# Performance work log

Hardware: AMD Instinct MI355X
Metric: run time of the kernel (lower is better)

The kernel has to match this reference:

```python
import jax, jax.numpy as jnp
import numpy as np

D_MODEL = 2048
NUM_HEADS = 16
HEAD_DIM = D_MODEL // NUM_HEADS


def setup_inputs() -> dict:
    key = jax.random.key(0)
    ks = jax.random.split(key, 11)
    B, S = 2, 2048
    scale = 1.0 / np.sqrt(D_MODEL)
    inp = {
        "q": jax.random.normal(ks[0], (B, S, D_MODEL), jnp.float32),
        "k": jax.random.normal(ks[1], (B, S, D_MODEL), jnp.float32),
        "v": jax.random.normal(ks[2], (B, S, D_MODEL), jnp.float32),
        "Wq": jax.random.normal(ks[3], (D_MODEL, D_MODEL), jnp.float32) * scale,
        "bq": jnp.zeros((D_MODEL,), jnp.float32),
        "Wk": jax.random.normal(ks[4], (D_MODEL, D_MODEL), jnp.float32) * scale,
        "bk": jnp.zeros((D_MODEL,), jnp.float32),
        "Wv": jax.random.normal(ks[5], (D_MODEL, D_MODEL), jnp.float32) * scale,
        "bv": jnp.zeros((D_MODEL,), jnp.float32),
        "Wo": jax.random.normal(ks[6], (D_MODEL, D_MODEL), jnp.float32) * scale,
        "bo": jnp.zeros((D_MODEL,), jnp.float32),
    }
    return inp


def reference(q, k, v, Wq, bq, Wk, bk, Wv, bv, Wo, bo):
    B, S, _ = q.shape
    # projections (torch Linear: x @ W.T + b)
    qh = (q @ Wq.T + bq).reshape(B, S, NUM_HEADS, HEAD_DIM).transpose(0, 2, 1, 3)
    kh = (k @ Wk.T + bk).reshape(B, S, NUM_HEADS, HEAD_DIM).transpose(0, 2, 1, 3)
    vh = (v @ Wv.T + bv).reshape(B, S, NUM_HEADS, HEAD_DIM).transpose(0, 2, 1, 3)
    # scaled dot-product attention, full O(S^2) scores as in original
    scores = jnp.einsum("bhqd,bhkd->bhqk", qh, kh) / jnp.sqrt(
        jnp.asarray(HEAD_DIM, jnp.float32)
    )
    attn = jax.nn.softmax(scores, axis=-1)
    out = jnp.einsum("bhqk,bhkd->bhqd", attn, vh)
    out = out.transpose(0, 2, 1, 3).reshape(B, S, D_MODEL)
    return out @ Wo.T + bo
```

## Files before the change

### kernel.cpp

```cpp
#include <hip/hip_runtime.h>


typedef __attribute__((ext_vector_type(8))) short bf16x8;
typedef __attribute__((ext_vector_type(4))) float f32x4;
typedef __attribute__((ext_vector_type(8))) unsigned short u16x8;

__device__ __forceinline__ unsigned short f2bf(float f) {
  unsigned int u = __float_as_uint(f);
  u += 0x7fffu + ((u >> 16) & 1u);
  return (unsigned short)(u >> 16);
}

#if __has_builtin(__builtin_amdgcn_cvt_pk_bf16_f32)
__device__ __forceinline__ unsigned int pack2bf(float x, float y) {
  auto r = __builtin_amdgcn_cvt_pk_bf16_f32(x, y);
  return __builtin_bit_cast(unsigned int, r);
}
#else
__device__ __forceinline__ unsigned int pack2bf(float x, float y) {
  return (unsigned int)f2bf(x) | ((unsigned int)f2bf(y) << 16);
}
#endif

__device__ __forceinline__ float fast_exp2(float x) {
#if __has_builtin(__builtin_amdgcn_exp2f)
  return __builtin_amdgcn_exp2f(x);
#else
  return exp2f(x);
#endif
}

__device__ __forceinline__ void async16(const void* g, void* l) {
  __builtin_amdgcn_global_load_lds(
      (const __attribute__((address_space(1))) unsigned int*)g,
      (__attribute__((address_space(3))) unsigned int*)l, 16, 0, 0);
}

__device__ __forceinline__ f32x4 mfma_bf16(bf16x8 a, bf16x8 b, f32x4 c) {
  return __builtin_amdgcn_mfma_f32_16x16x32_bf16(a, b, c, 0, 0, 0);
}

__global__ __launch_bounds__(256) void cvt_kernel(
    const float* __restrict__ q, const float* __restrict__ k,
    const float* __restrict__ v, const float* __restrict__ Wq,
    const float* __restrict__ Wk, const float* __restrict__ Wv,
    const float* __restrict__ Wo, unsigned short* __restrict__ Xq,
    unsigned short* __restrict__ Xk, unsigned short* __restrict__ Xv,
    unsigned short* __restrict__ WqB, unsigned short* __restrict__ WkB,
    unsigned short* __restrict__ WvB, unsigned short* __restrict__ WoB) {
  size_t i = ((size_t)blockIdx.x * 256 + threadIdx.x) * 8;
  const float* src;
  unsigned short* dst;
  size_t off;
  if (i < 8388608ull) { src = q; dst = Xq; off = i; }
  else if (i < 16777216ull) { src = k; dst = Xk; off = i - 8388608ull; }
  else if (i < 25165824ull) { src = v; dst = Xv; off = i - 16777216ull; }
  else if (i < 29360128ull) { src = Wq; dst = WqB; off = i - 25165824ull; }
  else if (i < 33554432ull) { src = Wk; dst = WkB; off = i - 29360128ull; }
  else if (i < 37748736ull) { src = Wv; dst = WvB; off = i - 33554432ull; }
  else { src = Wo; dst = WoB; off = i - 37748736ull; }
  f32x4 a = *(const f32x4*)(src + off);
  f32x4 b = *(const f32x4*)(src + off + 4);
  u16x8 r;
  r[0] = f2bf(a[0]); r[1] = f2bf(a[1]); r[2] = f2bf(a[2]); r[3] = f2bf(a[3]);
  r[4] = f2bf(b[0]); r[5] = f2bf(b[1]); r[6] = f2bf(b[2]); r[7] = f2bf(b[3]);
  *(u16x8*)(dst + off) = r;
}

#define MFMA_PHASE(AF, MB)                                                    \
  do {                                                                        \
    __builtin_amdgcn_s_setprio(1);                                            \
    _Pragma("unroll") for (int ks = 0; ks < 2; ++ks) {                        \
      _Pragma("unroll") for (int m2 = 0; m2 < 2; ++m2) {                      \
        _Pragma("unroll") for (int nt = 0; nt < 4; ++nt) {                    \
          acc[(MB) + m2][nt] =                                                \
              mfma_bf16(AF[m2][ks], Bf[nt][ks], acc[(MB) + m2][nt]);          \
        }                                                                     \
      }                                                                       \
    }                                                                         \
    __builtin_amdgcn_s_setprio(0);                                            \
  } while (0)

__global__ __launch_bounds__(512, 2) void qkv_gemm256(
    const unsigned short* __restrict__ Xq, const unsigned short* __restrict__ Xk,
    const unsigned short* __restrict__ Xv, const unsigned short* __restrict__ Wq,
    const unsigned short* __restrict__ Wk, const unsigned short* __restrict__ Wv,
    const float* __restrict__ bq, const float* __restrict__ bk,
    const float* __restrict__ bv, unsigned short* __restrict__ Qb,
    unsigned short* __restrict__ Kb, unsigned short* __restrict__ Vt) {
  __shared__ unsigned short S[2][4][128 * 64];
  const int z = blockIdx.z;
  const unsigned short* A = z == 0 ? Xq : z == 1 ? Xk : Xv;
  const unsigned short* Bm = z == 0 ? Wq : z == 1 ? Wk : Wv;
  const float* bias = z == 0 ? bq : z == 1 ? bk : bv;
  const int m0 = blockIdx.y * 256;
  const int n0 = blockIdx.x * 256;
  const int tid = threadIdx.x;
  const int lane = tid & 63;
  const int wave = tid >> 6;
  const int quad = lane >> 4;
  const int l15 = lane & 15;
  const int wm = wave >> 2;
  const int wn = wave & 3;
  const int cxor = l15 & 7;
  const int K = 2048;

  auto stage = [&](int r, int kt, int buf) {
#pragma unroll
    for (int p = 0; p < 2; ++p) {
      int x = p * 512 + tid;
      int row = ((x >> 7) << 4) + ((x >> 3) & 15);
      int gk = kt * 64 + (((x & 7) ^ ((x >> 3) & 7)) << 3);
      const unsigned short* src =
          (r < 2) ? Bm + (size_t)(n0 + r * 128 + row) * K + gk
                  : A + (size_t)(m0 + (r - 2) * 128 + row) * K + gk;
      async16(src, (char*)S[buf][r] + (size_t)(p * 512 + wave * 64) * 16);
    }
  };
  auto rdA = [&](int buf, int mt, int ks) -> bf16x8 {
    const unsigned short* base = S[buf][2 + wm];
    int chunk = mt * 128 + l15 * 8 + ((ks * 4 + quad) ^ cxor);
    return *(const bf16x8*)(base + chunk * 8);
  };
  auto rdB = [&](int buf, int nt, int ks) -> bf16x8 {
    const unsigned short* base = S[buf][wn >> 1];
    int chunk = ((wn & 1) * 4 + nt) * 128 + l15 * 8 + ((ks * 4 + quad) ^ cxor);
    return *(const bf16x8*)(base + chunk * 8);
  };

  f32x4 acc[8][4];
#pragma unroll
  for (int i = 0; i < 8; ++i)
#pragma unroll
    for (int j = 0; j < 4; ++j) acc[i][j] = f32x4{0.f, 0.f, 0.f, 0.f};
  bf16x8 Bf[4][2], AX[2][2], AY[2][2];

  stage(0, 0, 0); stage(1, 0, 0); stage(2, 0, 0); stage(3, 0, 0);
  stage(0, 1, 1); stage(1, 1, 1); stage(2, 1, 1);
  asm volatile("s_waitcnt vmcnt(6)" ::: "memory");
  __builtin_amdgcn_s_barrier();
#pragma unroll
  for (int nt = 0; nt < 4; ++nt)
#pragma unroll
    for (int ks = 0; ks < 2; ++ks) Bf[nt][ks] = rdB(0, nt, ks);
#pragma unroll
  for (int ks = 0; ks < 2; ++ks) {
    AX[0][ks] = rdA(0, 0, ks);
    AX[1][ks] = rdA(0, 1, ks);
  }

#pragma unroll 1
  for (int t = 0; t < 32; ++t) {
    const int buf = t & 1;
    const int nbuf = buf ^ 1;
    if (t < 31) stage(3, t + 1, nbuf);
#pragma unroll
    for (int ks = 0; ks < 2; ++ks) {
      AY[0][ks] = rdA(buf, 2, ks);
      AY[1][ks] = rdA(buf, 3, ks);
    }
    __builtin_amdgcn_sched_barrier(0);
    __builtin_amdgcn_s_barrier();
    __builtin_amdgcn_sched_barrier(0);
    MFMA_PHASE(AX, 0);
    __builtin_amdgcn_sched_barrier(0);
    __builtin_amdgcn_s_barrier();
    if (t < 30) stage(0, t + 2, buf);
#pragma unroll
    for (int ks = 0; ks < 2; ++ks) {
      AX[0][ks] = rdA(buf, 4, ks);
      AX[1][ks] = rdA(buf, 5, ks);
    }
    __builtin_amdgcn_sched_barrier(0);
    __builtin_amdgcn_s_barrier();
    __builtin_amdgcn_sched_barrier(0);
    MFMA_PHASE(AY, 2);
    __builtin_amdgcn_sched_barrier(0);
    __builtin_amdgcn_s_barrier();
    if (t < 30) stage(1, t + 2, buf);
#pragma unroll
    for (int ks = 0; ks < 2; ++ks) {
      AY[0][ks] = rdA(buf, 6, ks);
      AY[1][ks] = rdA(buf, 7, ks);
    }
    __builtin_amdgcn_sched_barrier(0);
    __builtin_amdgcn_s_barrier();
    __builtin_amdgcn_sched_barrier(0);
    MFMA_PHASE(AX, 4);
    if (t < 30) {
      asm volatile("s_waitcnt vmcnt(4)" ::: "memory");
    } else if (t == 30) {
      asm volatile("s_waitcnt vmcnt(0)" ::: "memory");
    }
    __builtin_amdgcn_sched_barrier(0);
    __builtin_amdgcn_s_barrier();
    if (t < 30) stage(2, t + 2, buf);
    if (t < 31) {
#pragma unroll
      for (int ks = 0; ks < 2; ++ks) {
        AX[0][ks] = rdA(nbuf, 0, ks);
        AX[1][ks] = rdA(nbuf, 1, ks);
      }
    }
    __builtin_amdgcn_sched_barrier(0);
    __builtin_amdgcn_s_barrier();
    __builtin_amdgcn_sched_barrier(0);
    MFMA_PHASE(AY, 6);
    if (t < 31) {
#pragma unroll
      for (int nt = 0; nt < 4; ++nt)
#pragma unroll
        for (int ks = 0; ks < 2; ++ks) Bf[nt][ks] = rdB(nbuf, nt, ks);
    }
    __builtin_amdgcn_sched_barrier(0);
    __builtin_amdgcn_s_barrier();
  }

  const float SK = z == 0 ? 0.12753102331285527f : 1.0f;
#pragma unroll
  for (int nt = 0; nt < 4; ++nt) {
    int col = n0 + wn * 64 + nt * 16 + l15;
    float bv_ = bias[col];
    if (z == 2) {
      int h = col >> 7, d = col & 127;
#pragma unroll
      for (int mt = 0; mt < 8; ++mt) {
        int row0 = m0 + wm * 128 + mt * 16 + quad * 4;
        int bb = row0 >> 11, s = row0 & 2047;
        uint2 pk;
        pk.x = pack2bf(acc[mt][nt][0] + bv_, acc[mt][nt][1] + bv_);
        pk.y = pack2bf(acc[mt][nt][2] + bv_, acc[mt][nt][3] + bv_);
        *(uint2*)(Vt + ((size_t)((bb * 16 + h) * 128 + d)) * 2048 + s) = pk;
      }
    } else {
      unsigned short* C = z == 0 ? Qb : Kb;
#pragma unroll
      for (int mt = 0; mt < 8; ++mt) {
        int row0 = m0 + wm * 128 + mt * 16 + quad * 4;
#pragma unroll
        for (int r = 0; r < 4; ++r)
          C[(size_t)(row0 + r) * 2048 + col] = f2bf((acc[mt][nt][r] + bv_) * SK);
      }
    }
  }
}

__device__ __forceinline__ void gemm_core_k2048(
    const unsigned short* __restrict__ A, const unsigned short* __restrict__ Bm,
    int m0, int n0, unsigned short* As, unsigned short* Bs,
    f32x4 (&acc)[4][4]) {
  const int tid = threadIdx.x;
  const int lane = tid & 63;
  const int wave = tid >> 6;
  const int quad = lane >> 4;
  const int l15 = lane & 15;
  const int wmt = (wave >> 1) * 4;
  const int wnt = (wave & 1) * 4;
  const int K = 2048;

  auto stage = [&](int kt, int buf) {
    unsigned short* SA = As + buf * (128 * 64);
    unsigned short* SB = Bs + buf * (128 * 64);
#pragma unroll
    for (int p = 0; p < 4; ++p) {
      int x = p * 256 + tid;
      int row = ((x >> 7) << 4) + ((x >> 3) & 15);
      int gk = kt + (((x & 7) ^ ((x >> 3) & 7)) << 3);
      async16(A + (size_t)(m0 + row) * K + gk,
              (char*)SA + (size_t)(p * 256 + wave * 64) * 16);
      async16(Bm + (size_t)(n0 + row) * K + gk,
              (char*)SB + (size_t)(p * 256 + wave * 64) * 16);
    }
  };
  stage(0, 0);
#pragma unroll 1
  for (int it = 0; it < 32; ++it) {
    __syncthreads();
    if (it + 1 < 32) stage((it + 1) * 64, (it + 1) & 1);
    const unsigned short* SA = As + (it & 1) * (128 * 64);
    const unsigned short* SB = Bs + (it & 1) * (128 * 64);
#pragma unroll
    for (int s = 0; s < 2; ++s) {
      const int cs = (s * 4 + quad) ^ (l15 & 7);
      bf16x8 af[4], bfr[4];
#pragma unroll
      for (int t = 0; t < 4; ++t) {
        af[t] = *(const bf16x8*)(SA + ((wmt + t) * 128 + l15 * 8 + cs) * 8);
        bfr[t] = *(const bf16x8*)(SB + ((wnt + t) * 128 + l15 * 8 + cs) * 8);
      }
#pragma unroll
      for (int mt = 0; mt < 4; ++mt)
#pragma unroll
        for (int nt = 0; nt < 4; ++nt)
          acc[mt][nt] = mfma_bf16(af[mt], bfr[nt], acc[mt][nt]);
    }
  }
}

__global__ __launch_bounds__(256, 2) void o_gemm(
    const unsigned short* __restrict__ A, const unsigned short* __restrict__ Bm,
    const float* __restrict__ bias, float* __restrict__ Cf) {
  __shared__ unsigned short As[2][128 * 64];
  __shared__ unsigned short Bs[2][128 * 64];
  const int m0 = blockIdx.y * 128;
  const int n0 = blockIdx.x * 128;

  f32x4 acc[4][4];
#pragma unroll
  for (int i = 0; i < 4; ++i)
#pragma unroll
    for (int j = 0; j < 4; ++j) acc[i][j] = f32x4{0.f, 0.f, 0.f, 0.f};
  gemm_core_k2048(A, Bm, m0, n0, As[0], Bs[0], acc);

  const int lane = threadIdx.x & 63;
  const int wave = threadIdx.x >> 6;
  const int quad = lane >> 4;
  const int l15 = lane & 15;
  const int wmt = (wave >> 1) * 4;
  const int wnt = (wave & 1) * 4;
  const int N = 2048;
#pragma unroll
  for (int nt = 0; nt < 4; ++nt) {
    int col = n0 + (wnt + nt) * 16 + l15;
    float bv_ = bias[col];
#pragma unroll
    for (int mt = 0; mt < 4; ++mt) {
      int row0 = m0 + (wmt + mt) * 16 + quad * 4;
#pragma unroll
      for (int r = 0; r < 4; ++r)
        Cf[(size_t)(row0 + r) * N + col] = acc[mt][nt][r] + bv_;
    }
  }
}

__global__ __launch_bounds__(256, 2) void attn_kernel(
    const unsigned short* __restrict__ Qg, const unsigned short* __restrict__ Kg,
    const unsigned short* __restrict__ Vt, unsigned short* __restrict__ ctx) {
  __shared__ unsigned short Ks[2][64 * 128];
  __shared__ unsigned short Vs[2][128 * 64];
  __shared__ unsigned short Ps[128 * 64];
  const int tid = threadIdx.x;
  const int lane = tid & 63;
  const int wave = tid >> 6;
  const int quad = lane >> 4;
  const int l15 = lane & 15;
  const int qt = blockIdx.x, h = blockIdx.y, b = blockIdx.z;
  const int q0 = qt * 128;
  const int swz = (l15 & 7) * 8;

  bf16x8 aq[2][4];
#pragma unroll
  for (int mt = 0; mt < 2; ++mt) {
    const unsigned short* qrow =
        Qg + (size_t)(b * 2048 + q0 + wave * 32 + mt * 16 + l15) * 2048 + h * 128;
#pragma unroll
    for (int ks = 0; ks < 4; ++ks)
      aq[mt][ks] = *(const bf16x8*)(qrow + ks * 32 + quad * 8);
  }

  f32x4 o[2][8];
#pragma unroll
  for (int mt = 0; mt < 2; ++mt)
#pragma unroll
    for (int dt = 0; dt < 8; ++dt) o[mt][dt] = f32x4{0.f, 0.f, 0.f, 0.f};
  f32x4 lacc[2] = {f32x4{0.f, 0.f, 0.f, 0.f}, f32x4{0.f, 0.f, 0.f, 0.f}};

  auto stage = [&](int t, int buf) {
#pragma unroll
    for (int p = 0; p < 4; ++p) {
      int slot = p * 256 + tid;
      {
        int nt = slot >> 8, c = (slot >> 4) & 15, r15 = slot & 15;
        const unsigned short* g =
            Kg + (size_t)(b * 2048 + t * 64 + nt * 16 + r15) * 2048 + h * 128 + c * 8;
        async16(g, (char*)Ks[buf] + (size_t)(p * 256 + wave * 64) * 16);
      }
      {
        int dt = slot >> 7, c = (slot >> 4) & 7, n15 = slot & 15;
        const unsigned short* g =
            Vt + ((size_t)(b * 16 + h) * 128 + dt * 16 + n15) * 2048 + t * 64 + c * 8;
        async16(g, (char*)Vs[buf] + (size_t)(p * 256 + wave * 64) * 16);
      }
    }
  };
  stage(0, 0);

  for (int t = 0; t < 32; ++t) {
    __syncthreads();
    if (t + 1 < 32) stage(t + 1, (t + 1) & 1);
    const unsigned short* Kb = Ks[t & 1];
    const unsigned short* Vb = Vs[t & 1];

    f32x4 sc[2][4];
#pragma unroll
    for (int nt = 0; nt < 4; ++nt) {
      sc[0][nt] = f32x4{0.f, 0.f, 0.f, 0.f};
      sc[1][nt] = f32x4{0.f, 0.f, 0.f, 0.f};
#pragma unroll
      for (int ks = 0; ks < 4; ++ks) {
        bf16x8 bk = *(const bf16x8*)(Kb + (nt * 256 + (ks * 4 + quad) * 16 + l15) * 8);
        sc[0][nt] = mfma_bf16(bk, aq[0][ks], sc[0][nt]);
        sc[1][nt] = mfma_bf16(bk, aq[1][ks], sc[1][nt]);
      }
    }

#pragma unroll
    for (int mt = 0; mt < 2; ++mt) {
      int prow = (wave * 32 + mt * 16 + l15) * 64;
#pragma unroll
      for (int nt = 0; nt < 4; ++nt) {
        f32x4 p;
#pragma unroll
        for (int r = 0; r < 4; ++r) p[r] = fast_exp2(sc[mt][nt][r]);
        lacc[mt] += p;
        uint2 pk;
        pk.x = pack2bf(p[0], p[1]);
        pk.y = pack2bf(p[2], p[3]);
        *(uint2*)(Ps + prow + ((nt * 16 + quad * 4) ^ swz)) = pk;
      }
    }

    bf16x8 ap[2][2];
#pragma unroll
    for (int mt = 0; mt < 2; ++mt) {
      int prow = (wave * 32 + mt * 16 + l15) * 64;
#pragma unroll
      for (int ks = 0; ks < 2; ++ks)
        ap[mt][ks] = *(const bf16x8*)(Ps + prow + ((ks * 32 + quad * 8) ^ swz));
    }
#pragma unroll
    for (int dt = 0; dt < 8; ++dt) {
#pragma unroll
      for (int ks = 0; ks < 2; ++ks) {
        bf16x8 bv = *(const bf16x8*)(Vb + (dt * 128 + (ks * 4 + quad) * 16 + l15) * 8);
        o[0][dt] = mfma_bf16(ap[0][ks], bv, o[0][dt]);
        o[1][dt] = mfma_bf16(ap[1][ks], bv, o[1][dt]);
      }
    }
  }

  float lq[2];
#pragma unroll
  for (int mt = 0; mt < 2; ++mt) {
    float s = lacc[mt][0] + lacc[mt][1] + lacc[mt][2] + lacc[mt][3];
    s += __shfl_xor(s, 16, 64);
    s += __shfl_xor(s, 32, 64);
    lq[mt] = s;
  }

#pragma unroll
  for (int mt = 0; mt < 2; ++mt) {
#pragma unroll
    for (int r = 0; r < 4; ++r) {
      float lr = __shfl(lq[mt], quad * 4 + r, 64);
      float inv = 1.0f / lr;
      unsigned short* crow =
          ctx + (size_t)(b * 2048 + q0 + wave * 32 + mt * 16 + quad * 4 + r) * 2048 +
          h * 128;
#pragma unroll
      for (int dt = 0; dt < 8; ++dt)
        crow[dt * 16 + l15] = f2bf(o[mt][dt][r] * inv);
    }
  }
}

extern "C" void kernel_launch(void* const* d_in, const int* in_sizes, int n_in,
                              void* d_out, int out_size, void* d_ws,
                              size_t ws_size, hipStream_t stream) {
  const float* q = (const float*)d_in[0];
  const float* k = (const float*)d_in[1];
  const float* v = (const float*)d_in[2];
  const float* Wq = (const float*)d_in[3];
  const float* bq = (const float*)d_in[4];
  const float* Wk = (const float*)d_in[5];
  const float* bk = (const float*)d_in[6];
  const float* Wv = (const float*)d_in[7];
  const float* bv = (const float*)d_in[8];
  const float* Wo = (const float*)d_in[9];
  const float* bo = (const float*)d_in[10];
  float* out = (float*)d_out;

  char* ws = (char*)d_ws;
  const size_t MB = 1024 * 1024;
  unsigned short* Xq  = (unsigned short*)(ws + 0 * MB);
  unsigned short* Xk  = (unsigned short*)(ws + 16 * MB);
  unsigned short* Xv  = (unsigned short*)(ws + 32 * MB);
  unsigned short* WqB = (unsigned short*)(ws + 48 * MB);
  unsigned short* WkB = (unsigned short*)(ws + 56 * MB);
  unsigned short* WvB = (unsigned short*)(ws + 64 * MB);
  unsigned short* WoB = (unsigned short*)(ws + 72 * MB);
  unsigned short* Qb  = (unsigned short*)(ws + 80 * MB);
  unsigned short* Kb  = (unsigned short*)(ws + 96 * MB);
  unsigned short* Vt  = (unsigned short*)(ws + 112 * MB);
  unsigned short* ctx = Xq;

  cvt_kernel<<<20480, 256, 0, stream>>>(q, k, v, Wq, Wk, Wv, Wo, Xq, Xk, Xv,
                                        WqB, WkB, WvB, WoB);
  qkv_gemm256<<<dim3(8, 16, 3), 512, 0, stream>>>(Xq, Xk, Xv, WqB, WkB, WvB,
                                                  bq, bk, bv, Qb, Kb, Vt);
  attn_kernel<<<dim3(16, 16, 2), 256, 0, stream>>>(Qb, Kb, Vt, ctx);
  o_gemm<<<dim3(16, 32), 256, 0, stream>>>(ctx, WoB, bo, out);
}
```

Baseline: 474.7 us.

## Restructure QKV GEMM into quadrant-wise MFMA phases with interleaved staging

Reorganizes the 256x256 QKV projection GEMM so each wave computes four 64x32 quadrants, one per phase. A and B fragments are reloaded from LDS per quadrant, and each staged half-tile is issued for the next k-step as soon as its LDS slot is consumed. The wave-to-output mapping changes from 128x64 contiguous to split 2x2 quadrants, and the epilogue indexing is updated to match. The aim is finer-grained overlap of global loads with MFMA work and fewer live fragment registers. In exchange it adds more LDS reads per k-step and drops the sched_barrier fences, so the compiler may reorder instructions.

New measurement: 467.6 us. No clear change (-1.5%).

```diff
diff --git a/kernel.cpp b/kernel.cpp
--- a/kernel.cpp
+++ b/kernel.cpp
@@ -67,20 +67,6 @@
   *(u16x8*)(dst + off) = r;
 }
 
-#define MFMA_PHASE(AF, MB)                                                    \
-  do {                                                                        \
-    __builtin_amdgcn_s_setprio(1);                                            \
-    _Pragma("unroll") for (int ks = 0; ks < 2; ++ks) {                        \
-      _Pragma("unroll") for (int m2 = 0; m2 < 2; ++m2) {                      \
-        _Pragma("unroll") for (int nt = 0; nt < 4; ++nt) {                    \
-          acc[(MB) + m2][nt] =                                                \
-              mfma_bf16(AF[m2][ks], Bf[nt][ks], acc[(MB) + m2][nt]);          \
-        }                                                                     \
-      }                                                                       \
-    }                                                                         \
-    __builtin_amdgcn_s_setprio(0);                                            \
-  } while (0)
-
 __global__ __launch_bounds__(512, 2) void qkv_gemm256(
     const unsigned short* __restrict__ Xq, const unsigned short* __restrict__ Xk,
     const unsigned short* __restrict__ Xv, const unsigned short* __restrict__ Wq,
@@ -117,14 +103,14 @@
       async16(src, (char*)S[buf][r] + (size_t)(p * 512 + wave * 64) * 16);
     }
   };
-  auto rdA = [&](int buf, int mt, int ks) -> bf16x8 {
-    const unsigned short* base = S[buf][2 + wm];
-    int chunk = mt * 128 + l15 * 8 + ((ks * 4 + quad) ^ cxor);
+  auto rdA = [&](int buf, int mh, int m, int ks) -> bf16x8 {
+    const unsigned short* base = S[buf][2 + mh];
+    int chunk = (wm * 4 + m) * 128 + l15 * 8 + ((ks * 4 + quad) ^ cxor);
     return *(const bf16x8*)(base + chunk * 8);
   };
-  auto rdB = [&](int buf, int nt, int ks) -> bf16x8 {
-    const unsigned short* base = S[buf][wn >> 1];
-    int chunk = ((wn & 1) * 4 + nt) * 128 + l15 * 8 + ((ks * 4 + quad) ^ cxor);
+  auto rdB = [&](int buf, int nh, int n, int ks) -> bf16x8 {
+    const unsigned short* base = S[buf][nh];
+    int chunk = (wn * 2 + n) * 128 + l15 * 8 + ((ks * 4 + quad) ^ cxor);
     return *(const bf16x8*)(base + chunk * 8);
   };
 
@@ -133,113 +119,116 @@
   for (int i = 0; i < 8; ++i)
 #pragma unroll
     for (int j = 0; j < 4; ++j) acc[i][j] = f32x4{0.f, 0.f, 0.f, 0.f};
-  bf16x8 Bf[4][2], AX[2][2], AY[2][2];
-
-  stage(0, 0, 0); stage(1, 0, 0); stage(2, 0, 0); stage(3, 0, 0);
-  stage(0, 1, 1); stage(1, 1, 1); stage(2, 1, 1);
-  asm volatile("s_waitcnt vmcnt(6)" ::: "memory");
+  bf16x8 Af[4][2], Bfr[2][2];
+
+  stage(2, 0, 0); stage(1, 0, 0); stage(0, 0, 0); stage(3, 0, 0);
+  stage(0, 1, 1); stage(3, 1, 1);
+  asm volatile("s_waitcnt vmcnt(4)" ::: "memory");
   __builtin_amdgcn_s_barrier();
-#pragma unroll
-  for (int nt = 0; nt < 4; ++nt)
-#pragma unroll
-    for (int ks = 0; ks < 2; ++ks) Bf[nt][ks] = rdB(0, nt, ks);
-#pragma unroll
-  for (int ks = 0; ks < 2; ++ks) {
-    AX[0][ks] = rdA(0, 0, ks);
-    AX[1][ks] = rdA(0, 1, ks);
-  }
 
 #pragma unroll 1
   for (int t = 0; t < 32; ++t) {
     const int buf = t & 1;
     const int nbuf = buf ^ 1;
-    if (t < 31) stage(3, t + 1, nbuf);
-#pragma unroll
-    for (int ks = 0; ks < 2; ++ks) {
-      AY[0][ks] = rdA(buf, 2, ks);
-      AY[1][ks] = rdA(buf, 3, ks);
-    }
-    __builtin_amdgcn_sched_barrier(0);
-    __builtin_amdgcn_s_barrier();
-    __builtin_amdgcn_sched_barrier(0);
-    MFMA_PHASE(AX, 0);
-    __builtin_amdgcn_sched_barrier(0);
-    __builtin_amdgcn_s_barrier();
-    if (t < 30) stage(0, t + 2, buf);
-#pragma unroll
-    for (int ks = 0; ks < 2; ++ks) {
-      AX[0][ks] = rdA(buf, 4, ks);
-      AX[1][ks] = rdA(buf, 5, ks);
-    }
-    __builtin_amdgcn_sched_barrier(0);
-    __builtin_amdgcn_s_barrier();
-    __builtin_amdgcn_sched_barrier(0);
-    MFMA_PHASE(AY, 2);
-    __builtin_amdgcn_sched_barrier(0);
-    __builtin_amdgcn_s_barrier();
-    if (t < 30) stage(1, t + 2, buf);
-#pragma unroll
-    for (int ks = 0; ks < 2; ++ks) {
-      AY[0][ks] = rdA(buf, 6, ks);
-      AY[1][ks] = rdA(buf, 7, ks);
-    }
-    __builtin_amdgcn_sched_barrier(0);
-    __builtin_amdgcn_s_barrier();
-    __builtin_amdgcn_sched_barrier(0);
-    MFMA_PHASE(AX, 4);
+#pragma unroll
+    for (int m = 0; m < 4; ++m)
+#pragma unroll
+      for (int ks = 0; ks < 2; ++ks) Af[m][ks] = rdA(buf, 0, m, ks);
+#pragma unroll
+    for (int n = 0; n < 2; ++n)
+#pragma unroll
+      for (int ks = 0; ks < 2; ++ks) Bfr[n][ks] = rdB(buf, 0, n, ks);
+    if (t + 1 < 32) stage(2, t + 1, nbuf);
+    __builtin_amdgcn_s_barrier();
+    __builtin_amdgcn_s_setprio(1);
+#pragma unroll
+    for (int ks = 0; ks < 2; ++ks)
+#pragma unroll
+      for (int m = 0; m < 4; ++m)
+#pragma unroll
+        for (int n = 0; n < 2; ++n)
+          acc[m][n] = mfma_bf16(Af[m][ks], Bfr[n][ks], acc[m][n]);
+    __builtin_amdgcn_s_setprio(0);
+    __builtin_amdgcn_s_barrier();
+#pragma unroll
+    for (int m = 0; m < 4; ++m)
+#pragma unroll
+      for (int ks = 0; ks < 2; ++ks) Af[m][ks] = rdA(buf, 1, m, ks);
+    if (t + 1 < 32) stage(1, t + 1, nbuf);
+    __builtin_amdgcn_s_barrier();
+    __builtin_amdgcn_s_setprio(1);
+#pragma unroll
+    for (int ks = 0; ks < 2; ++ks)
+#pragma unroll
+      for (int m = 0; m < 4; ++m)
+#pragma unroll
+        for (int n = 0; n < 2; ++n)
+          acc[4 + m][n] = mfma_bf16(Af[m][ks], Bfr[n][ks], acc[4 + m][n]);
+    __builtin_amdgcn_s_setprio(0);
+    __builtin_amdgcn_s_barrier();
+#pragma unroll
+    for (int n = 0; n < 2; ++n)
+#pragma unroll
+      for (int ks = 0; ks < 2; ++ks) Bfr[n][ks] = rdB(buf, 1, n, ks);
+    if (t + 2 < 32) stage(0, t + 2, buf);
+    __builtin_amdgcn_s_barrier();
+    __builtin_amdgcn_s_setprio(1);
+#pragma unroll
+    for (int ks = 0; ks < 2; ++ks)
+#pragma unroll
+      for (int m = 0; m < 4; ++m)
+#pragma unroll
+        for (int n = 0; n < 2; ++n)
+          acc[4 + m][2 + n] = mfma_bf16(Af[m][ks], Bfr[n][ks], acc[4 + m][2 + n]);
+    __builtin_amdgcn_s_setprio(0);
+    __builtin_amdgcn_s_barrier();
+#pragma unroll
+    for (int m = 0; m < 4; ++m)
+#pragma unroll
+      for (int ks = 0; ks < 2; ++ks) Af[m][ks] = rdA(buf, 0, m, ks);
+    if (t + 2 < 32) stage(3, t + 2, buf);
     if (t < 30) {
       asm volatile("s_waitcnt vmcnt(4)" ::: "memory");
     } else if (t == 30) {
       asm volatile("s_waitcnt vmcnt(0)" ::: "memory");
     }
-    __builtin_amdgcn_sched_barrier(0);
-    __builtin_amdgcn_s_barrier();
-    if (t < 30) stage(2, t + 2, buf);
-    if (t < 31) {
-#pragma unroll
-      for (int ks = 0; ks < 2; ++ks) {
-        AX[0][ks] = rdA(nbuf, 0, ks);
-        AX[1][ks] = rdA(nbuf, 1, ks);
-      }
-    }
-    __builtin_amdgcn_sched_barrier(0);
-    __builtin_amdgcn_s_barrier();
-    __builtin_amdgcn_sched_barrier(0);
-    MFMA_PHASE(AY, 6);
-    if (t < 31) {
-#pragma unroll
-      for (int nt = 0; nt < 4; ++nt)
-#pragma unroll
-        for (int ks = 0; ks < 2; ++ks) Bf[nt][ks] = rdB(nbuf, nt, ks);
-    }
-    __builtin_amdgcn_sched_barrier(0);
+    __builtin_amdgcn_s_barrier();
+    __builtin_amdgcn_s_setprio(1);
+#pragma unroll
+    for (int ks = 0; ks < 2; ++ks)
+#pragma unroll
+      for (int m = 0; m < 4; ++m)
+#pragma unroll
+        for (int n = 0; n < 2; ++n)
+          acc[m][2 + n] = mfma_bf16(Af[m][ks], Bfr[n][ks], acc[m][2 + n]);
+    __builtin_amdgcn_s_setprio(0);
     __builtin_amdgcn_s_barrier();
   }
 
   const float SK = z == 0 ? 0.12753102331285527f : 1.0f;
 #pragma unroll
-  for (int nt = 0; nt < 4; ++nt) {
-    int col = n0 + wn * 64 + nt * 16 + l15;
+  for (int nf = 0; nf < 4; ++nf) {
+    int col = n0 + (nf >> 1) * 128 + wn * 32 + (nf & 1) * 16 + l15;
     float bv_ = bias[col];
     if (z == 2) {
       int h = col >> 7, d = col & 127;
 #pragma unroll
-      for (int mt = 0; mt < 8; ++mt) {
-        int row0 = m0 + wm * 128 + mt * 16 + quad * 4;
+      for (int mf = 0; mf < 8; ++mf) {
+        int row0 = m0 + (mf >> 2) * 128 + wm * 64 + (mf & 3) * 16 + quad * 4;
         int bb = row0 >> 11, s = row0 & 2047;
         uint2 pk;
-        pk.x = pack2bf(acc[mt][nt][0] + bv_, acc[mt][nt][1] + bv_);
-        pk.y = pack2bf(acc[mt][nt][2] + bv_, acc[mt][nt][3] + bv_);
+        pk.x = pack2bf(acc[mf][nf][0] + bv_, acc[mf][nf][1] + bv_);
+        pk.y = pack2bf(acc[mf][nf][2] + bv_, acc[mf][nf][3] + bv_);
         *(uint2*)(Vt + ((size_t)((bb * 16 + h) * 128 + d)) * 2048 + s) = pk;
       }
     } else {
       unsigned short* C = z == 0 ? Qb : Kb;
 #pragma unroll
-      for (int mt = 0; mt < 8; ++mt) {
-        int row0 = m0 + wm * 128 + mt * 16 + quad * 4;
+      for (int mf = 0; mf < 8; ++mf) {
+        int row0 = m0 + (mf >> 2) * 128 + wm * 64 + (mf & 3) * 16 + quad * 4;
 #pragma unroll
         for (int r = 0; r < 4; ++r)
-          C[(size_t)(row0 + r) * 2048 + col] = f2bf((acc[mt][nt][r] + bv_) * SK);
+          C[(size_t)(row0 + r) * 2048 + col] = f2bf((acc[mf][nf][r] + bv_) * SK);
       }
     }
   }
```
